# Optimization experiments

Measured on AMD Instinct MI355X. Metric: run time of the kernel, lower is better.

Reference implementation:

```python
import jax, jax.numpy as jnp
import numpy as np

ARTIST_V = 16384
GENRE_V = 2048
TOTAL = ARTIST_V + GENRE_V + 1  # 18433
HIDDEN = TOTAL // 2            # 9216
OUT = 64
BATCH = 4096


def setup_inputs() -> dict:
    key = jax.random.key(0)
    k1, k2, k3, k4, k5, k6, k7 = jax.random.split(key, 7)
    artist_ids = jax.random.randint(k1, (BATCH,), 0, ARTIST_V, dtype=jnp.int64 if jax.config.jax_enable_x64 else jnp.int32)
    genre_ids = jax.random.randint(k2, (BATCH,), 0, GENRE_V, dtype=artist_ids.dtype)
    year_norms = jax.random.uniform(k3, (BATCH,), dtype=jnp.float32)
    s1 = 1.0 / np.sqrt(TOTAL)
    s2 = 1.0 / np.sqrt(HIDDEN)
    W1 = jax.random.uniform(k4, (HIDDEN, TOTAL), jnp.float32, -s1, s1)
    b1 = jax.random.uniform(k5, (HIDDEN,), jnp.float32, -s1, s1)
    W2 = jax.random.uniform(k6, (OUT, HIDDEN), jnp.float32, -s2, s2)
    b2 = jax.random.uniform(k7, (OUT,), jnp.float32, -s2, s2)
    return {"artist_ids": artist_ids, "genre_ids": genre_ids, "year_norms": year_norms,
            "W1": W1, "b1": b1, "W2": W2, "b2": b2}


def reference(artist_ids, genre_ids, year_norms, W1, b1, W2, b2):
    # one_hot(artist) @ W1[:, :A].T  ==  gather of W1 columns == gather of W1.T rows.
    # combined = [onehot(artist) | onehot(genre) | year] -> Linear -> ReLU -> Linear
    # (Dropout is identity at inference.)
    W1T = W1.T  # [TOTAL, HIDDEN]
    h = (W1T[artist_ids]                     # [B, HIDDEN] artist one-hot matmul
         + W1T[ARTIST_V + genre_ids]         # genre one-hot matmul
         + year_norms[:, None] * W1T[-1]     # year scalar column
         + b1)
    h = jax.nn.relu(h)
    return h @ W2.T + b2  # [B, OUT]
```

## Files before the change

### kernel.cpp

```cpp
#include <hip/hip_runtime.h>

#define ARTIST_V 16384
#define GENRE_V  2048
#define TOTAL    18433
#define HIDDEN   9216
#define OUT_D    64
#define BATCH    4096

#define ROWS_PB  6
#define NBLK     (HIDDEN / ROWS_PB)
#define THR      512
#define SEG      (TOTAL - 1)
#define PF_N     (SEG / 4 / THR)

#define KSPLIT   4
#define KCHUNK   (HIDDEN / KSPLIT)

typedef unsigned int   uint;
typedef unsigned short ushort;
typedef __attribute__((ext_vector_type(8))) short short8;
typedef __attribute__((ext_vector_type(4))) float f32x4;

__device__ __forceinline__ ushort f2bf(float f) {
    uint u = __float_as_uint(f);
    u += 0x7FFFu + ((u >> 16) & 1u);
    return (ushort)(u >> 16);
}
__device__ __forceinline__ float bf2f(ushort b) {
    return __uint_as_float(((uint)b) << 16);
}

__global__ __launch_bounds__(256) void k_prep(const float* __restrict__ W2,
                                              ushort* __restrict__ W2b) {
    int t = blockIdx.x * 256 + threadIdx.x;
    float4 v = *(const float4*)(W2 + (size_t)t * 4);
    uint2 p;
    p.x = (uint)f2bf(v.x) | ((uint)f2bf(v.y) << 16);
    p.y = (uint)f2bf(v.z) | ((uint)f2bf(v.w) << 16);
    *(uint2*)(W2b + (size_t)t * 4) = p;
}

__global__ __launch_bounds__(THR) void k_hidden(
    const int*   __restrict__ artist,
    const int*   __restrict__ genre,
    const float* __restrict__ year,
    const float* __restrict__ W1,
    const float* __restrict__ b1,
    uint*        __restrict__ H2p)
{
    __shared__ ushort srow[SEG];
    const int tid = threadIdx.x;
    const int hb  = blockIdx.x;
    const int h0  = hb * ROWS_PB;

    uint  ag[8]; float yv[8];
    #pragma unroll
    for (int j = 0; j < 8; j++) {
        int b = tid + THR * j;
        ag[j] = (uint)artist[b] | ((uint)genre[b] << 16);
        yv[j] = year[b];
    }

    uint res[8][3];
    #pragma unroll
    for (int j = 0; j < 8; j++) { res[j][0] = 0u; res[j][1] = 0u; res[j][2] = 0u; }

    float4 pf[PF_N];
    {
        const float4* vp = (const float4*)(W1 + (size_t)h0 * TOTAL);
        #pragma unroll
        for (int i = 0; i < PF_N; i++) pf[i] = vp[i * THR + tid];
        #pragma unroll
        for (int i = 0; i < PF_N; i++) {
            uint2 p;
            p.x = (uint)f2bf(pf[i].x) | ((uint)f2bf(pf[i].y) << 16);
            p.y = (uint)f2bf(pf[i].z) | ((uint)f2bf(pf[i].w) << 16);
            *(uint2*)(srow + (i * THR + tid) * 4) = p;
        }
        __syncthreads();
    }

    #pragma unroll
    for (int r = 0; r < ROWS_PB; r++) {
        const int h = h0 + r;
        if (r + 1 < ROWS_PB) {
            const float4* vp = (const float4*)(W1 + (size_t)(h + 1) * TOTAL);
            #pragma unroll
            for (int i = 0; i < PF_N; i++) pf[i] = vp[i * THR + tid];
        }
        const float yw  = W1[(size_t)h * TOTAL + SEG];
        const float b1h = b1[h];
        #pragma unroll
        for (int j = 0; j < 8; j++) {
            int a = (int)(ag[j] & 0xFFFFu);
            int g = (int)(ag[j] >> 16);
            float hv = bf2f(srow[a]) + bf2f(srow[ARTIST_V + g]) + yv[j] * yw + b1h;
            hv = fmaxf(hv, 0.0f);
            res[j][r >> 1] |= ((uint)f2bf(hv)) << ((r & 1) * 16);
        }
        __syncthreads();
        if (r + 1 < ROWS_PB) {
            #pragma unroll
            for (int i = 0; i < PF_N; i++) {
                uint2 p;
                p.x = (uint)f2bf(pf[i].x) | ((uint)f2bf(pf[i].y) << 16);
                p.y = (uint)f2bf(pf[i].z) | ((uint)f2bf(pf[i].w) << 16);
                *(uint2*)(srow + (i * THR + tid) * 4) = p;
            }
            __syncthreads();
        }
    }

    #pragma unroll
    for (int q = 0; q < 3; q++) {
        size_t base = (size_t)(hb * 3 + q) * BATCH;
        #pragma unroll
        for (int j = 0; j < 8; j++) H2p[base + tid + THR * j] = res[j][q];
    }
}

__global__ __launch_bounds__(256) void k_gemm(
    const uint*   __restrict__ H2p,
    const ushort* __restrict__ W2b,
    float*        __restrict__ part)
{
    const int lane = threadIdx.x & 63;
    const int wv   = threadIdx.x >> 6;
    const int l15  = lane & 15;
    const int lhi  = lane >> 4;
    const int m0   = blockIdx.x * 64 + wv * 16;
    const int k0   = blockIdx.y * KCHUNK;

    f32x4 acc[4];
    #pragma unroll
    for (int n = 0; n < 4; n++) acc[n] = (f32x4){0.f, 0.f, 0.f, 0.f};

    for (int kk = k0; kk < k0 + KCHUNK; kk += 32) {
        int p0 = (kk >> 1) + lhi * 4;
        union { uint u[4]; short8 s; } ua;
        #pragma unroll
        for (int q = 0; q < 4; q++)
            ua.u[q] = H2p[(size_t)(p0 + q) * BATCH + m0 + l15];
        short8 afrag = ua.s;

        const ushort* wb = W2b + (size_t)l15 * HIDDEN + kk + lhi * 8;
        #pragma unroll
        for (int n = 0; n < 4; n++) {
            short8 bfrag = *(const short8*)(wb + (size_t)(n * 16) * HIDDEN);
            acc[n] = __builtin_amdgcn_mfma_f32_16x16x32_bf16(afrag, bfrag, acc[n], 0, 0, 0);
        }
    }

    float* pb = part + (size_t)blockIdx.y * (BATCH * OUT_D);
    #pragma unroll
    for (int n = 0; n < 4; n++) {
        #pragma unroll
        for (int r = 0; r < 4; r++)
            pb[(size_t)(m0 + lhi * 4 + r) * OUT_D + n * 16 + l15] = acc[n][r];
    }
}

__global__ __launch_bounds__(256) void k_reduce(const float* __restrict__ part,
                                                const float* __restrict__ b2,
                                                float4*      __restrict__ out4) {
    int idx = blockIdx.x * 256 + threadIdx.x;
    const float4* p = (const float4*)part;
    float4 s0 = p[idx];
    float4 s1 = p[idx + 65536];
    float4 s2 = p[idx + 131072];
    float4 s3 = p[idx + 196608];
    float4 bb = ((const float4*)b2)[threadIdx.x & 15];
    float4 o;
    o.x = s0.x + s1.x + s2.x + s3.x + bb.x;
    o.y = s0.y + s1.y + s2.y + s3.y + bb.y;
    o.z = s0.z + s1.z + s2.z + s3.z + bb.z;
    o.w = s0.w + s1.w + s2.w + s3.w + bb.w;
    out4[idx] = o;
}

extern "C" void kernel_launch(void* const* d_in, const int* in_sizes, int n_in,
                              void* d_out, int out_size, void* d_ws, size_t ws_size,
                              hipStream_t stream) {
    const int*   artist = (const int*)d_in[0];
    const int*   genre  = (const int*)d_in[1];
    const float* year   = (const float*)d_in[2];
    const float* W1     = (const float*)d_in[3];
    const float* b1     = (const float*)d_in[4];
    const float* W2     = (const float*)d_in[5];
    const float* b2     = (const float*)d_in[6];
    float* out = (float*)d_out;

    char* ws = (char*)d_ws;
    uint*   H2p = (uint*)ws;
    ushort* W2b = (ushort*)(ws + 75497472);
    float*  part = (float*)(ws + 75497472 + 1179648);

    k_prep  <<<576, 256, 0, stream>>>(W2, W2b);
    k_hidden<<<NBLK, THR, 0, stream>>>(artist, genre, year, W1, b1, H2p);
    k_gemm  <<<dim3(BATCH / 64, KSPLIT), 256, 0, stream>>>(H2p, W2b, part);
    k_reduce<<<256, 256, 0, stream>>>(part, b2, (float4*)out);
}
```

Before: 941.3 us.

## Double-buffer hidden LDS rows, pack 8 rows per uint4, widen GEMM K-split

The hidden kernel now handles 8 W1 rows per block and stores its bf16 outputs as uint4 (8 hidden values per batch element). Its LDS row is double-buffered, so one barrier per row is removed, and the year-weight and bias loads are hoisted up front. The GEMM reads one uint4 per lane with a one-step register prefetch and uses K-split 8, and the reduce loops over the splits. Float-to-bf16 conversion uses the packed v_cvt_pk_bf16_f32 instruction, and occupancy hints are added. Risks include higher register pressure in k_hidden, fewer blocks (1152) there, and twice the partial-sum traffic in the reduce.

```diff
diff --git a/kernel.cpp b/kernel.cpp
--- a/kernel.cpp
+++ b/kernel.cpp
@@ -7,13 +7,13 @@
 #define OUT_D    64
 #define BATCH    4096
 
-#define ROWS_PB  6
+#define ROWS_PB  8
 #define NBLK     (HIDDEN / ROWS_PB)
 #define THR      512
 #define SEG      (TOTAL - 1)
 #define PF_N     (SEG / 4 / THR)
 
-#define KSPLIT   4
+#define KSPLIT   8
 #define KCHUNK   (HIDDEN / KSPLIT)
 
 typedef unsigned int   uint;
@@ -28,6 +28,11 @@
 }
 __device__ __forceinline__ float bf2f(ushort b) {
     return __uint_as_float(((uint)b) << 16);
+}
+__device__ __forceinline__ uint cvt_pk(float a, float b) {
+    uint r;
+    asm("v_cvt_pk_bf16_f32 %0, %1, %2" : "=v"(r) : "v"(a), "v"(b));
+    return r;
 }
 
 __global__ __launch_bounds__(256) void k_prep(const float* __restrict__ W2,
@@ -35,20 +40,20 @@
     int t = blockIdx.x * 256 + threadIdx.x;
     float4 v = *(const float4*)(W2 + (size_t)t * 4);
     uint2 p;
-    p.x = (uint)f2bf(v.x) | ((uint)f2bf(v.y) << 16);
-    p.y = (uint)f2bf(v.z) | ((uint)f2bf(v.w) << 16);
+    p.x = cvt_pk(v.x, v.y);
+    p.y = cvt_pk(v.z, v.w);
     *(uint2*)(W2b + (size_t)t * 4) = p;
 }
 
-__global__ __launch_bounds__(THR) void k_hidden(
+__global__ __launch_bounds__(THR, 4) void k_hidden(
     const int*   __restrict__ artist,
     const int*   __restrict__ genre,
     const float* __restrict__ year,
     const float* __restrict__ W1,
     const float* __restrict__ b1,
-    uint*        __restrict__ H2p)
+    uint4*       __restrict__ H2v)
 {
-    __shared__ ushort srow[SEG];
+    __shared__ ushort srow[2][SEG];
     const int tid = threadIdx.x;
     const int hb  = blockIdx.x;
     const int h0  = hb * ROWS_PB;
@@ -60,10 +65,17 @@
         ag[j] = (uint)artist[b] | ((uint)genre[b] << 16);
         yv[j] = year[b];
     }
-
-    uint res[8][3];
-    #pragma unroll
-    for (int j = 0; j < 8; j++) { res[j][0] = 0u; res[j][1] = 0u; res[j][2] = 0u; }
+    float ywA[ROWS_PB], b1A[ROWS_PB];
+    #pragma unroll
+    for (int r = 0; r < ROWS_PB; r++) {
+        ywA[r] = W1[(size_t)(h0 + r) * TOTAL + SEG];
+        b1A[r] = b1[h0 + r];
+    }
+
+    uint res[8][4];
+    #pragma unroll
+    for (int j = 0; j < 8; j++)
+        { res[j][0] = 0u; res[j][1] = 0u; res[j][2] = 0u; res[j][3] = 0u; }
 
     float4 pf[PF_N];
     {
@@ -72,55 +84,50 @@
         for (int i = 0; i < PF_N; i++) pf[i] = vp[i * THR + tid];
         #pragma unroll
         for (int i = 0; i < PF_N; i++) {
-            uint2 p;
-            p.x = (uint)f2bf(pf[i].x) | ((uint)f2bf(pf[i].y) << 16);
-            p.y = (uint)f2bf(pf[i].z) | ((uint)f2bf(pf[i].w) << 16);
-            *(uint2*)(srow + (i * THR + tid) * 4) = p;
+            uint2 p; p.x = cvt_pk(pf[i].x, pf[i].y); p.y = cvt_pk(pf[i].z, pf[i].w);
+            *(uint2*)(&srow[0][(i * THR + tid) * 4]) = p;
         }
         __syncthreads();
     }
 
     #pragma unroll
     for (int r = 0; r < ROWS_PB; r++) {
-        const int h = h0 + r;
         if (r + 1 < ROWS_PB) {
-            const float4* vp = (const float4*)(W1 + (size_t)(h + 1) * TOTAL);
+            const float4* vp = (const float4*)(W1 + (size_t)(h0 + r + 1) * TOTAL);
             #pragma unroll
             for (int i = 0; i < PF_N; i++) pf[i] = vp[i * THR + tid];
         }
-        const float yw  = W1[(size_t)h * TOTAL + SEG];
-        const float b1h = b1[h];
+        const ushort* sr = srow[r & 1];
+        const float yw = ywA[r], bh = b1A[r];
         #pragma unroll
         for (int j = 0; j < 8; j++) {
             int a = (int)(ag[j] & 0xFFFFu);
             int g = (int)(ag[j] >> 16);
-            float hv = bf2f(srow[a]) + bf2f(srow[ARTIST_V + g]) + yv[j] * yw + b1h;
+            float hv = bf2f(sr[a]) + bf2f(sr[ARTIST_V + g]) + yv[j] * yw + bh;
             hv = fmaxf(hv, 0.0f);
             res[j][r >> 1] |= ((uint)f2bf(hv)) << ((r & 1) * 16);
         }
-        __syncthreads();
         if (r + 1 < ROWS_PB) {
+            ushort* sw = srow[(r + 1) & 1];
             #pragma unroll
             for (int i = 0; i < PF_N; i++) {
-                uint2 p;
-                p.x = (uint)f2bf(pf[i].x) | ((uint)f2bf(pf[i].y) << 16);
-                p.y = (uint)f2bf(pf[i].z) | ((uint)f2bf(pf[i].w) << 16);
-                *(uint2*)(srow + (i * THR + tid) * 4) = p;
+                uint2 p; p.x = cvt_pk(pf[i].x, pf[i].y); p.y = cvt_pk(pf[i].z, pf[i].w);
+                *(uint2*)(&sw[(i * THR + tid) * 4]) = p;
             }
             __syncthreads();
         }
     }
 
-    #pragma unroll
-    for (int q = 0; q < 3; q++) {
-        size_t base = (size_t)(hb * 3 + q) * BATCH;
-        #pragma unroll
-        for (int j = 0; j < 8; j++) H2p[base + tid + THR * j] = res[j][q];
-    }
-}
-
-__global__ __launch_bounds__(256) void k_gemm(
-    const uint*   __restrict__ H2p,
+    const size_t obase = (size_t)hb * BATCH;
+    #pragma unroll
+    for (int j = 0; j < 8; j++) {
+        uint4 v; v.x = res[j][0]; v.y = res[j][1]; v.z = res[j][2]; v.w = res[j][3];
+        H2v[obase + tid + THR * j] = v;
+    }
+}
+
+__global__ __launch_bounds__(256, 2) void k_gemm(
+    const uint4*  __restrict__ H2v,
     const ushort* __restrict__ W2b,
     float*        __restrict__ part)
 {
@@ -135,12 +142,12 @@
     #pragma unroll
     for (int n = 0; n < 4; n++) acc[n] = (f32x4){0.f, 0.f, 0.f, 0.f};
 
+    uint4 avn = H2v[(size_t)((k0 >> 3) + lhi) * BATCH + m0 + l15];
     for (int kk = k0; kk < k0 + KCHUNK; kk += 32) {
-        int p0 = (kk >> 1) + lhi * 4;
-        union { uint u[4]; short8 s; } ua;
-        #pragma unroll
-        for (int q = 0; q < 4; q++)
-            ua.u[q] = H2p[(size_t)(p0 + q) * BATCH + m0 + l15];
+        uint4 av = avn;
+        if (kk + 32 < k0 + KCHUNK)
+            avn = H2v[(size_t)(((kk + 32) >> 3) + lhi) * BATCH + m0 + l15];
+        union { uint4 u; short8 s; } ua; ua.u = av;
         short8 afrag = ua.s;
 
         const ushort* wb = W2b + (size_t)l15 * HIDDEN + kk + lhi * 8;
@@ -165,16 +172,13 @@
                                                 float4*      __restrict__ out4) {
     int idx = blockIdx.x * 256 + threadIdx.x;
     const float4* p = (const float4*)part;
-    float4 s0 = p[idx];
-    float4 s1 = p[idx + 65536];
-    float4 s2 = p[idx + 131072];
-    float4 s3 = p[idx + 196608];
     float4 bb = ((const float4*)b2)[threadIdx.x & 15];
-    float4 o;
-    o.x = s0.x + s1.x + s2.x + s3.x + bb.x;
-    o.y = s0.y + s1.y + s2.y + s3.y + bb.y;
-    o.z = s0.z + s1.z + s2.z + s3.z + bb.z;
-    o.w = s0.w + s1.w + s2.w + s3.w + bb.w;
+    float4 o = bb;
+    #pragma unroll
+    for (int s = 0; s < KSPLIT; s++) {
+        float4 v = p[idx + (size_t)s * 65536];
+        o.x += v.x; o.y += v.y; o.z += v.z; o.w += v.w;
+    }
     out4[idx] = o;
 }
 
@@ -191,12 +195,12 @@
     float* out = (float*)d_out;
 
     char* ws = (char*)d_ws;
-    uint*   H2p = (uint*)ws;
-    ushort* W2b = (ushort*)(ws + 75497472);
+    uint4*  H2v  = (uint4*)ws;
+    ushort* W2b  = (ushort*)(ws + 75497472);
     float*  part = (float*)(ws + 75497472 + 1179648);
 
     k_prep  <<<576, 256, 0, stream>>>(W2, W2b);
-    k_hidden<<<NBLK, THR, 0, stream>>>(artist, genre, year, W1, b1, H2p);
-    k_gemm  <<<dim3(BATCH / 64, KSPLIT), 256, 0, stream>>>(H2p, W2b, part);
+    k_hidden<<<NBLK, THR, 0, stream>>>(artist, genre, year, W1, b1, H2v);
+    k_gemm  <<<dim3(BATCH / 64, KSPLIT), 256, 0, stream>>>(H2v, W2b, part);
     k_reduce<<<256, 256, 0, stream>>>(part, b2, (float4*)out);
 }
```

New measurement: 957.7 us. Within noise of the previous version (+1.7%).
